# Performance work log

Measured on AMD Instinct MI355X. Metric: run time of the kernel, lower is better.

Reference implementation:

```python
import jax, jax.numpy as jnp
import numpy as np

IN, H1, H2, V = 1024, 2048, 2048, 50257


def setup_inputs() -> dict:
    key = jax.random.key(0)
    ks = jax.random.split(key, 16)
    def n(k, shape, scale=1.0):
        return (jax.random.normal(k, shape, dtype=jnp.float32) * scale).astype(jnp.float32)
    s1 = 1.0 / np.sqrt(H1)  # pytorch LSTM init scale ~ U(-1/sqrt(H),1/sqrt(H)); gaussian stand-in
    s2 = 1.0 / np.sqrt(H2)
    so = 1.0 / np.sqrt(H2)
    return {
        "x":  n(ks[0], (IN,)),
        "h1": n(ks[1], (H1,)), "c1": n(ks[2], (H1,)),
        "h2": n(ks[3], (H2,)), "c2": n(ks[4], (H2,)),
        "W_ih1": n(ks[5], (4 * H1, IN), s1), "W_hh1": n(ks[6], (4 * H1, H1), s1),
        "b_ih1": n(ks[7], (4 * H1,), s1),   "b_hh1": n(ks[8], (4 * H1,), s1),
        "W_ih2": n(ks[9], (4 * H2, H1), s2), "W_hh2": n(ks[10], (4 * H2, H2), s2),
        "b_ih2": n(ks[11], (4 * H2,), s2),  "b_hh2": n(ks[12], (4 * H2,), s2),
        "W_out": n(ks[13], (V, H2), so),    "b_out": n(ks[14], (V,), so),
    }


def _lstm_step(x, h, c, W_ih, W_hh, b_ih, b_hh):
    # PyTorch gate ordering: i, f, g, o
    gates = W_ih @ x + b_ih + W_hh @ h + b_hh  # [4H]
    i, f, g, o = jnp.split(gates, 4)
    i = jax.nn.sigmoid(i)
    f = jax.nn.sigmoid(f)
    g = jnp.tanh(g)
    o = jax.nn.sigmoid(o)
    c_new = f * c + i * g
    h_new = o * jnp.tanh(c_new)
    return h_new, c_new


def reference(x, h1, c1, h2, c2,
              W_ih1, W_hh1, b_ih1, b_hh1,
              W_ih2, W_hh2, b_ih2, b_hh2,
              W_out, b_out):
    h1n, _ = _lstm_step(x, h1, c1, W_ih1, W_hh1, b_ih1, b_hh1)
    h2n, _ = _lstm_step(h1n, h2, c2, W_ih2, W_hh2, b_ih2, b_hh2)
    logits = W_out @ h2n + b_out                     # [V]
    # dropout(p=0.1) treated as identity (eval mode) for a deterministic baseline
    return jax.nn.log_softmax(logits)[None, :]       # [1, V], matches dim=1 log-softmax
```

## Files before the change

### kernel.cpp

```cpp
#include <hip/hip_runtime.h>
#include <hip/hip_bf16.h>

typedef unsigned short u16;
typedef u16 u16x8 __attribute__((ext_vector_type(8)));
typedef float f32x8 __attribute__((ext_vector_type(8)));

#define IN_DIM 1024
#define H_DIM  2048
#define V_DIM  50257
#define NEG_BIG (-1e30f)

__device__ __forceinline__ float bf2f(u16 u) {
    union { unsigned int i; float f; } v;
    v.i = ((unsigned int)u) << 16;
    return v.f;
}

__device__ __forceinline__ u16 f2bf(float f) {
    union { float f; unsigned int i; } v;
    v.f = f;
    unsigned int i = v.i;
    i += 0x7fffu + ((i >> 16) & 1u);
    return (u16)(i >> 16);
}

__device__ __forceinline__ float wave_reduce_sum(float v) {
    #pragma unroll
    for (int off = 32; off > 0; off >>= 1) v += __shfl_down(v, off, 64);
    return v;
}

__device__ __forceinline__ float sigmoidf(float x) { return 1.f / (1.f + __expf(-x)); }

__device__ __forceinline__ float ld_scalar(const void* p, int i, bool bf) {
    return bf ? bf2f(((const u16*)p)[i]) : ((const float*)p)[i];
}

__device__ __forceinline__ const void* row_ptr(const void* W, size_t row, int n, bool bf) {
    return (const void*)((const char*)W + row * (size_t)n * (bf ? 2u : 4u));
}

template<int N>
__device__ __forceinline__ float dot_dt(const void* wrow, const void* v, int lane, bool bf) {
    float acc = 0.f;
    if (bf) {
        const u16x8* wp = (const u16x8*)wrow;
        const u16x8* vp = (const u16x8*)v;
        #pragma unroll
        for (int k = 0; k < N / 512; ++k) {
            u16x8 a = wp[lane + 64 * k];
            u16x8 b = vp[lane + 64 * k];
            #pragma unroll
            for (int t = 0; t < 8; ++t) acc += bf2f(a[t]) * bf2f(b[t]);
        }
    } else {
        const f32x8* wp = (const f32x8*)wrow;
        const f32x8* vp = (const f32x8*)v;
        #pragma unroll
        for (int k = 0; k < N / 512; ++k) {
            f32x8 a = wp[lane + 64 * k];
            f32x8 b = vp[lane + 64 * k];
            #pragma unroll
            for (int t = 0; t < 8; ++t) acc += a[t] * b[t];
        }
    }
    return acc;
}

template<int N>
__device__ __forceinline__ float dot_dt_f32v(const void* wrow, const float* v, int lane, bool bf) {
    float acc = 0.f;
    const f32x8* vp = (const f32x8*)v;
    if (bf) {
        const u16x8* wp = (const u16x8*)wrow;
        #pragma unroll
        for (int k = 0; k < N / 512; ++k) {
            u16x8 a = wp[lane + 64 * k];
            f32x8 b = vp[lane + 64 * k];
            #pragma unroll
            for (int t = 0; t < 8; ++t) acc += bf2f(a[t]) * b[t];
        }
    } else {
        const f32x8* wp = (const f32x8*)wrow;
        #pragma unroll
        for (int k = 0; k < N / 512; ++k) {
            f32x8 a = wp[lane + 64 * k];
            f32x8 b = vp[lane + 64 * k];
            #pragma unroll
            for (int t = 0; t < 8; ++t) acc += a[t] * b[t];
        }
    }
    return acc;
}

__global__ __launch_bounds__(64) void probe_kernel(const void* x, int* flag) {
    const int lane = threadIdx.x;
    const u16* p = (const u16*)x;
    int cnt = 0;
    #pragma unroll
    for (int k = 0; k < 8; ++k) {
        u16 w = p[2 * (lane + 64 * k)];
        int e = (w >> 7) & 0xFF;
        if (e >= 0x60 && e <= 0x8F) cnt++;
    }
    float c = wave_reduce_sum((float)cnt);
    if (lane == 0) flag[0] = (c > 300.f) ? 1 : 0;
}

__global__ __launch_bounds__(256) void lstm1_kernel(
    const void* __restrict__ x, const void* __restrict__ h1, const void* __restrict__ c1,
    const void* __restrict__ W_ih, const void* __restrict__ W_hh,
    const void* __restrict__ b_ih, const void* __restrict__ b_hh,
    const int* __restrict__ flag, float* __restrict__ h_out)
{
    const bool bf  = (*flag != 0);
    const int j    = blockIdx.x;
    const int wave = threadIdx.x >> 6;
    const int lane = threadIdx.x & 63;
    const int row  = wave * H_DIM + j;

    float acc = dot_dt<IN_DIM>(row_ptr(W_ih, (size_t)row, IN_DIM, bf), x, lane, bf)
              + dot_dt<H_DIM>(row_ptr(W_hh, (size_t)row, H_DIM, bf), h1, lane, bf);
    acc = wave_reduce_sum(acc);

    __shared__ float gs[4];
    if (lane == 0) gs[wave] = acc + ld_scalar(b_ih, row, bf) + ld_scalar(b_hh, row, bf);
    __syncthreads();
    if (threadIdx.x == 0) {
        float gi = sigmoidf(gs[0]);
        float gf = sigmoidf(gs[1]);
        float gg = tanhf(gs[2]);
        float go = sigmoidf(gs[3]);
        float c  = gf * ld_scalar(c1, j, bf) + gi * gg;
        h_out[j] = go * tanhf(c);
    }
}

__global__ __launch_bounds__(256) void lstm2_kernel(
    const float* __restrict__ h1n, const void* __restrict__ h2, const void* __restrict__ c2,
    const void* __restrict__ W_ih, const void* __restrict__ W_hh,
    const void* __restrict__ b_ih, const void* __restrict__ b_hh,
    const int* __restrict__ flag, float* __restrict__ h_out)
{
    const bool bf  = (*flag != 0);
    const int j    = blockIdx.x;
    const int wave = threadIdx.x >> 6;
    const int lane = threadIdx.x & 63;
    const int row  = wave * H_DIM + j;

    float acc = dot_dt_f32v<H_DIM>(row_ptr(W_ih, (size_t)row, H_DIM, bf), h1n, lane, bf)
              + dot_dt<H_DIM>(row_ptr(W_hh, (size_t)row, H_DIM, bf), h2, lane, bf);
    acc = wave_reduce_sum(acc);

    __shared__ float gs[4];
    if (lane == 0) gs[wave] = acc + ld_scalar(b_ih, row, bf) + ld_scalar(b_hh, row, bf);
    __syncthreads();
    if (threadIdx.x == 0) {
        float gi = sigmoidf(gs[0]);
        float gf = sigmoidf(gs[1]);
        float gg = tanhf(gs[2]);
        float go = sigmoidf(gs[3]);
        float c  = gf * ld_scalar(c2, j, bf) + gi * gg;
        h_out[j] = go * tanhf(c);
    }
}

#define ROWS_PER_WAVE 8
#define ROWS_PER_BLOCK 32
__global__ __launch_bounds__(256) void logits_kernel(
    const float* __restrict__ h2n, const void* __restrict__ W, const void* __restrict__ b,
    const int* __restrict__ flag,
    float* __restrict__ logits, float* __restrict__ pmax, float* __restrict__ psum)
{
    const bool bf  = (*flag != 0);
    const int wave = threadIdx.x >> 6;
    const int lane = threadIdx.x & 63;

    float hreg[32];
    {
        const f32x8* hv = (const f32x8*)h2n;
        #pragma unroll
        for (int k = 0; k < 4; ++k) {
            f32x8 hh = hv[lane + 64 * k];
            #pragma unroll
            for (int t = 0; t < 8; ++t) hreg[8 * k + t] = hh[t];
        }
    }

    const int base = blockIdx.x * ROWS_PER_BLOCK + wave * ROWS_PER_WAVE;
    float m = NEG_BIG, s = 0.f;
    for (int rr = 0; rr < ROWS_PER_WAVE; ++rr) {
        const int row = base + rr;
        if (row < V_DIM) {
            float acc = 0.f;
            if (bf) {
                const u16x8* wr = (const u16x8*)row_ptr(W, (size_t)row, H_DIM, true);
                #pragma unroll
                for (int k = 0; k < 4; ++k) {
                    u16x8 w = wr[lane + 64 * k];
                    #pragma unroll
                    for (int t = 0; t < 8; ++t) acc += bf2f(w[t]) * hreg[8 * k + t];
                }
            } else {
                const f32x8* wr = (const f32x8*)row_ptr(W, (size_t)row, H_DIM, false);
                #pragma unroll
                for (int k = 0; k < 4; ++k) {
                    f32x8 w = wr[lane + 64 * k];
                    #pragma unroll
                    for (int t = 0; t < 8; ++t) acc += w[t] * hreg[8 * k + t];
                }
            }
            acc = wave_reduce_sum(acc);
            if (lane == 0) {
                float lg = acc + ld_scalar(b, row, bf);
                logits[row] = lg;
                float mn = fmaxf(m, lg);
                s = s * __expf(m - mn) + __expf(lg - mn);
                m = mn;
            }
        }
    }
    __shared__ float wm[4], wsv[4];
    if (lane == 0) { wm[wave] = m; wsv[wave] = s; }
    __syncthreads();
    if (threadIdx.x == 0) {
        float M = fmaxf(fmaxf(wm[0], wm[1]), fmaxf(wm[2], wm[3]));
        float S = 0.f;
        #pragma unroll
        for (int w = 0; w < 4; ++w) S += wsv[w] * __expf(wm[w] - M);
        pmax[blockIdx.x] = M;
        psum[blockIdx.x] = S;
    }
}

__global__ __launch_bounds__(256) void finalize_kernel(
    const float* __restrict__ logits, const float* __restrict__ pmax,
    const float* __restrict__ psum, int nblk, const int* __restrict__ flag,
    void* __restrict__ out)
{
    const bool bf = (*flag != 0);
    __shared__ float sm[256], ss[256];
    float m = NEG_BIG, s = 0.f;
    for (int i = threadIdx.x; i < nblk; i += 256) {
        float bm = pmax[i], bs = psum[i];
        float mn = fmaxf(m, bm);
        s = s * __expf(m - mn) + bs * __expf(bm - mn);
        m = mn;
    }
    sm[threadIdx.x] = m; ss[threadIdx.x] = s;
    __syncthreads();
    #pragma unroll
    for (int stride = 128; stride > 0; stride >>= 1) {
        if ((int)threadIdx.x < stride) {
            float m1 = sm[threadIdx.x], s1 = ss[threadIdx.x];
            float m2 = sm[threadIdx.x + stride], s2 = ss[threadIdx.x + stride];
            float mn = fmaxf(m1, m2);
            sm[threadIdx.x] = mn;
            ss[threadIdx.x] = s1 * __expf(m1 - mn) + s2 * __expf(m2 - mn);
        }
        __syncthreads();
    }
    const float logZ = sm[0] + __logf(ss[0]);
    const int i = blockIdx.x * 256 + threadIdx.x;
    if (i < V_DIM) {
        float v = logits[i] - logZ;
        if (bf) ((u16*)out)[i] = f2bf(v);
        else    ((float*)out)[i] = v;
    }
}

extern "C" void kernel_launch(void* const* d_in, const int* in_sizes, int n_in,
                              void* d_out, int out_size, void* d_ws, size_t ws_size,
                              hipStream_t stream)
{
    const void* x     = d_in[0];
    const void* h1    = d_in[1];
    const void* c1    = d_in[2];
    const void* h2    = d_in[3];
    const void* c2    = d_in[4];
    const void* W_ih1 = d_in[5];
    const void* W_hh1 = d_in[6];
    const void* b_ih1 = d_in[7];
    const void* b_hh1 = d_in[8];
    const void* W_ih2 = d_in[9];
    const void* W_hh2 = d_in[10];
    const void* b_ih2 = d_in[11];
    const void* b_hh2 = d_in[12];
    const void* W_out = d_in[13];
    const void* b_out = d_in[14];

    float* ws     = (float*)d_ws;
    float* h1n    = ws;
    float* h2n    = ws + 2048;
    float* logits = ws + 4096;
    float* pmax   = ws + 4096 + 50264;
    float* psum   = pmax + 1576;
    int*   flag   = (int*)(psum + 1576);

    const int nblk3 = (V_DIM + ROWS_PER_BLOCK - 1) / ROWS_PER_BLOCK;

    probe_kernel<<<1, 64, 0, stream>>>(x, flag);
    lstm1_kernel<<<H_DIM, 256, 0, stream>>>(x, h1, c1, W_ih1, W_hh1, b_ih1, b_hh1, flag, h1n);
    lstm2_kernel<<<H_DIM, 256, 0, stream>>>(h1n, h2, c2, W_ih2, W_hh2, b_ih2, b_hh2, flag, h2n);
    logits_kernel<<<nblk3, 256, 0, stream>>>(h2n, W_out, b_out, flag, logits, pmax, psum);
    finalize_kernel<<<(V_DIM + 255) / 256, 256, 0, stream>>>(logits, pmax, psum, nblk3, flag, d_out);
}
```

Measured before the change: 679.0 us.

## Inline dtype probe, use nontemporal weight loads, batch two rows per wave in logits

Drops the separate probe kernel and has every block detect bf16 inline with a wave ballot, which saves one launch and the flag load that each kernel waited on. Weight rows are now read with nontemporal loads, all loads are issued before any math, and the logits kernel handles two rows per wave step with xor butterfly reductions so more memory requests are in flight. The row-bounds branches are replaced by clamped indices. The cost is a redundant probe read in every block, and the inline probe samples fewer elements, which makes the dtype guess less robust.

```diff
diff --git a/kernel.cpp b/kernel.cpp
--- a/kernel.cpp
+++ b/kernel.cpp
@@ -24,9 +24,12 @@
     return (u16)(i >> 16);
 }
 
-__device__ __forceinline__ float wave_reduce_sum(float v) {
+template<typename T>
+__device__ __forceinline__ T ntl(const T* p) { return __builtin_nontemporal_load(p); }
+
+__device__ __forceinline__ float wave_allreduce_sum(float v) {
     #pragma unroll
-    for (int off = 32; off > 0; off >>= 1) v += __shfl_down(v, off, 64);
+    for (int d = 32; d; d >>= 1) v += __shfl_xor(v, d, 64);
     return v;
 }
 
@@ -36,92 +39,76 @@
     return bf ? bf2f(((const u16*)p)[i]) : ((const float*)p)[i];
 }
 
-__device__ __forceinline__ const void* row_ptr(const void* W, size_t row, int n, bool bf) {
-    return (const void*)((const char*)W + row * (size_t)n * (bf ? 2u : 4u));
-}
-
-template<int N>
-__device__ __forceinline__ float dot_dt(const void* wrow, const void* v, int lane, bool bf) {
-    float acc = 0.f;
-    if (bf) {
-        const u16x8* wp = (const u16x8*)wrow;
-        const u16x8* vp = (const u16x8*)v;
-        #pragma unroll
-        for (int k = 0; k < N / 512; ++k) {
-            u16x8 a = wp[lane + 64 * k];
-            u16x8 b = vp[lane + 64 * k];
-            #pragma unroll
-            for (int t = 0; t < 8; ++t) acc += bf2f(a[t]) * bf2f(b[t]);
-        }
-    } else {
-        const f32x8* wp = (const f32x8*)wrow;
-        const f32x8* vp = (const f32x8*)v;
-        #pragma unroll
-        for (int k = 0; k < N / 512; ++k) {
-            f32x8 a = wp[lane + 64 * k];
-            f32x8 b = vp[lane + 64 * k];
-            #pragma unroll
-            for (int t = 0; t < 8; ++t) acc += a[t] * b[t];
-        }
-    }
-    return acc;
-}
-
-template<int N>
-__device__ __forceinline__ float dot_dt_f32v(const void* wrow, const float* v, int lane, bool bf) {
-    float acc = 0.f;
-    const f32x8* vp = (const f32x8*)v;
-    if (bf) {
-        const u16x8* wp = (const u16x8*)wrow;
-        #pragma unroll
-        for (int k = 0; k < N / 512; ++k) {
-            u16x8 a = wp[lane + 64 * k];
-            f32x8 b = vp[lane + 64 * k];
-            #pragma unroll
-            for (int t = 0; t < 8; ++t) acc += bf2f(a[t]) * b[t];
-        }
-    } else {
-        const f32x8* wp = (const f32x8*)wrow;
-        #pragma unroll
-        for (int k = 0; k < N / 512; ++k) {
-            f32x8 a = wp[lane + 64 * k];
-            f32x8 b = vp[lane + 64 * k];
-            #pragma unroll
-            for (int t = 0; t < 8; ++t) acc += a[t] * b[t];
-        }
-    }
-    return acc;
-}
-
-__global__ __launch_bounds__(64) void probe_kernel(const void* x, int* flag) {
-    const int lane = threadIdx.x;
+__device__ __forceinline__ bool probe_bf16(const void* x) {
     const u16* p = (const u16*)x;
-    int cnt = 0;
-    #pragma unroll
-    for (int k = 0; k < 8; ++k) {
-        u16 w = p[2 * (lane + 64 * k)];
-        int e = (w >> 7) & 0xFF;
-        if (e >= 0x60 && e <= 0x8F) cnt++;
-    }
-    float c = wave_reduce_sum((float)cnt);
-    if (lane == 0) flag[0] = (c > 300.f) ? 1 : 0;
+    const int lane = threadIdx.x & 63;
+    u16 w = p[2 * lane];
+    int e = (w >> 7) & 0xFF;
+    unsigned long long b = __ballot(e >= 0x60 && e <= 0x8F);
+    return __popcll(b) > 40;
 }
 
 __global__ __launch_bounds__(256) void lstm1_kernel(
     const void* __restrict__ x, const void* __restrict__ h1, const void* __restrict__ c1,
     const void* __restrict__ W_ih, const void* __restrict__ W_hh,
     const void* __restrict__ b_ih, const void* __restrict__ b_hh,
-    const int* __restrict__ flag, float* __restrict__ h_out)
-{
-    const bool bf  = (*flag != 0);
+    float* __restrict__ h_out)
+{
+    const bool bf  = probe_bf16(x);
     const int j    = blockIdx.x;
     const int wave = threadIdx.x >> 6;
     const int lane = threadIdx.x & 63;
     const int row  = wave * H_DIM + j;
 
-    float acc = dot_dt<IN_DIM>(row_ptr(W_ih, (size_t)row, IN_DIM, bf), x, lane, bf)
-              + dot_dt<H_DIM>(row_ptr(W_hh, (size_t)row, H_DIM, bf), h1, lane, bf);
-    acc = wave_reduce_sum(acc);
+    float acc = 0.f;
+    if (bf) {
+        {
+            const u16x8* wp = (const u16x8*)W_ih + (size_t)row * (IN_DIM / 8) + lane;
+            const u16x8* vp = (const u16x8*)x + lane;
+            u16x8 a[2], v[2];
+            #pragma unroll
+            for (int k = 0; k < 2; ++k) { a[k] = ntl(wp + 64 * k); v[k] = vp[64 * k]; }
+            #pragma unroll
+            for (int k = 0; k < 2; ++k)
+                #pragma unroll
+                for (int t = 0; t < 8; ++t) acc += bf2f(a[k][t]) * bf2f(v[k][t]);
+        }
+        {
+            const u16x8* wp = (const u16x8*)W_hh + (size_t)row * (H_DIM / 8) + lane;
+            const u16x8* vp = (const u16x8*)h1 + lane;
+            u16x8 a[4], v[4];
+            #pragma unroll
+            for (int k = 0; k < 4; ++k) { a[k] = ntl(wp + 64 * k); v[k] = vp[64 * k]; }
+            #pragma unroll
+            for (int k = 0; k < 4; ++k)
+                #pragma unroll
+                for (int t = 0; t < 8; ++t) acc += bf2f(a[k][t]) * bf2f(v[k][t]);
+        }
+    } else {
+        {
+            const f32x8* wp = (const f32x8*)W_ih + (size_t)row * (IN_DIM / 8) + lane;
+            const f32x8* vp = (const f32x8*)x + lane;
+            f32x8 a[2], v[2];
+            #pragma unroll
+            for (int k = 0; k < 2; ++k) { a[k] = ntl(wp + 64 * k); v[k] = vp[64 * k]; }
+            #pragma unroll
+            for (int k = 0; k < 2; ++k)
+                #pragma unroll
+                for (int t = 0; t < 8; ++t) acc += a[k][t] * v[k][t];
+        }
+        {
+            const f32x8* wp = (const f32x8*)W_hh + (size_t)row * (H_DIM / 8) + lane;
+            const f32x8* vp = (const f32x8*)h1 + lane;
+            f32x8 a[4], v[4];
+            #pragma unroll
+            for (int k = 0; k < 4; ++k) { a[k] = ntl(wp + 64 * k); v[k] = vp[64 * k]; }
+            #pragma unroll
+            for (int k = 0; k < 4; ++k)
+                #pragma unroll
+                for (int t = 0; t < 8; ++t) acc += a[k][t] * v[k][t];
+        }
+    }
+    acc = wave_allreduce_sum(acc);
 
     __shared__ float gs[4];
     if (lane == 0) gs[wave] = acc + ld_scalar(b_ih, row, bf) + ld_scalar(b_hh, row, bf);
@@ -137,20 +124,67 @@
 }
 
 __global__ __launch_bounds__(256) void lstm2_kernel(
+    const void* __restrict__ x,
     const float* __restrict__ h1n, const void* __restrict__ h2, const void* __restrict__ c2,
     const void* __restrict__ W_ih, const void* __restrict__ W_hh,
     const void* __restrict__ b_ih, const void* __restrict__ b_hh,
-    const int* __restrict__ flag, float* __restrict__ h_out)
-{
-    const bool bf  = (*flag != 0);
+    float* __restrict__ h_out)
+{
+    const bool bf  = probe_bf16(x);
     const int j    = blockIdx.x;
     const int wave = threadIdx.x >> 6;
     const int lane = threadIdx.x & 63;
     const int row  = wave * H_DIM + j;
 
-    float acc = dot_dt_f32v<H_DIM>(row_ptr(W_ih, (size_t)row, H_DIM, bf), h1n, lane, bf)
-              + dot_dt<H_DIM>(row_ptr(W_hh, (size_t)row, H_DIM, bf), h2, lane, bf);
-    acc = wave_reduce_sum(acc);
+    float acc = 0.f;
+    if (bf) {
+        {
+            const u16x8* wp = (const u16x8*)W_ih + (size_t)row * (H_DIM / 8) + lane;
+            const f32x8* vp = (const f32x8*)h1n + lane;
+            u16x8 a[4]; f32x8 v[4];
+            #pragma unroll
+            for (int k = 0; k < 4; ++k) { a[k] = ntl(wp + 64 * k); v[k] = vp[64 * k]; }
+            #pragma unroll
+            for (int k = 0; k < 4; ++k)
+                #pragma unroll
+                for (int t = 0; t < 8; ++t) acc += bf2f(a[k][t]) * v[k][t];
+        }
+        {
+            const u16x8* wp = (const u16x8*)W_hh + (size_t)row * (H_DIM / 8) + lane;
+            const u16x8* vp = (const u16x8*)h2 + lane;
+            u16x8 a[4], v[4];
+            #pragma unroll
+            for (int k = 0; k < 4; ++k) { a[k] = ntl(wp + 64 * k); v[k] = vp[64 * k]; }
+            #pragma unroll
+            for (int k = 0; k < 4; ++k)
+                #pragma unroll
+                for (int t = 0; t < 8; ++t) acc += bf2f(a[k][t]) * bf2f(v[k][t]);
+        }
+    } else {
+        {
+            const f32x8* wp = (const f32x8*)W_ih + (size_t)row * (H_DIM / 8) + lane;
+            const f32x8* vp = (const f32x8*)h1n + lane;
+            f32x8 a[4], v[4];
+            #pragma unroll
+            for (int k = 0; k < 4; ++k) { a[k] = ntl(wp + 64 * k); v[k] = vp[64 * k]; }
+            #pragma unroll
+            for (int k = 0; k < 4; ++k)
+                #pragma unroll
+                for (int t = 0; t < 8; ++t) acc += a[k][t] * v[k][t];
+        }
+        {
+            const f32x8* wp = (const f32x8*)W_hh + (size_t)row * (H_DIM / 8) + lane;
+            const f32x8* vp = (const f32x8*)h2 + lane;
+            f32x8 a[4], v[4];
+            #pragma unroll
+            for (int k = 0; k < 4; ++k) { a[k] = ntl(wp + 64 * k); v[k] = vp[64 * k]; }
+            #pragma unroll
+            for (int k = 0; k < 4; ++k)
+                #pragma unroll
+                for (int t = 0; t < 8; ++t) acc += a[k][t] * v[k][t];
+        }
+    }
+    acc = wave_allreduce_sum(acc);
 
     __shared__ float gs[4];
     if (lane == 0) gs[wave] = acc + ld_scalar(b_ih, row, bf) + ld_scalar(b_hh, row, bf);
@@ -168,11 +202,11 @@
 #define ROWS_PER_WAVE 8
 #define ROWS_PER_BLOCK 32
 __global__ __launch_bounds__(256) void logits_kernel(
+    const void* __restrict__ x,
     const float* __restrict__ h2n, const void* __restrict__ W, const void* __restrict__ b,
-    const int* __restrict__ flag,
     float* __restrict__ logits, float* __restrict__ pmax, float* __restrict__ psum)
 {
-    const bool bf  = (*flag != 0);
+    const bool bf  = probe_bf16(x);
     const int wave = threadIdx.x >> 6;
     const int lane = threadIdx.x & 63;
 
@@ -189,37 +223,73 @@
 
     const int base = blockIdx.x * ROWS_PER_BLOCK + wave * ROWS_PER_WAVE;
     float m = NEG_BIG, s = 0.f;
-    for (int rr = 0; rr < ROWS_PER_WAVE; ++rr) {
-        const int row = base + rr;
-        if (row < V_DIM) {
+
+    if (bf) {
+        #pragma unroll
+        for (int p = 0; p < 4; ++p) {
+            const int r0 = base + 2 * p, r1 = r0 + 1;
+            const int c0 = min(r0, V_DIM - 1), c1 = min(r1, V_DIM - 1);
+            const u16x8* w0 = (const u16x8*)W + (size_t)c0 * (H_DIM / 8) + lane;
+            const u16x8* w1 = (const u16x8*)W + (size_t)c1 * (H_DIM / 8) + lane;
+            u16x8 a0[4], a1[4];
+            #pragma unroll
+            for (int k = 0; k < 4; ++k) { a0[k] = ntl(w0 + 64 * k); a1[k] = ntl(w1 + 64 * k); }
+            float acc0 = 0.f, acc1 = 0.f;
+            #pragma unroll
+            for (int k = 0; k < 4; ++k)
+                #pragma unroll
+                for (int t = 0; t < 8; ++t) {
+                    float hval = hreg[8 * k + t];
+                    acc0 += bf2f(a0[k][t]) * hval;
+                    acc1 += bf2f(a1[k][t]) * hval;
+                }
+            #pragma unroll
+            for (int d = 32; d; d >>= 1) {
+                acc0 += __shfl_xor(acc0, d, 64);
+                acc1 += __shfl_xor(acc1, d, 64);
+            }
+            const float l0 = acc0 + ld_scalar(b, c0, true);
+            const float l1 = acc1 + ld_scalar(b, c1, true);
+            const bool v0 = (r0 < V_DIM), v1 = (r1 < V_DIM);
+            if (lane == 0) {
+                if (v0) logits[r0] = l0;
+                if (v1) logits[r1] = l1;
+            }
+            const float mx = fmaxf(v0 ? l0 : NEG_BIG, v1 ? l1 : NEG_BIG);
+            if (mx > -1e29f) {
+                const float mn = fmaxf(m, mx);
+                s = s * __expf(m - mn)
+                  + (v0 ? __expf(l0 - mn) : 0.f)
+                  + (v1 ? __expf(l1 - mn) : 0.f);
+                m = mn;
+            }
+        }
+    } else {
+        #pragma unroll
+        for (int rr = 0; rr < ROWS_PER_WAVE; ++rr) {
+            const int r = base + rr;
+            const int cr = min(r, V_DIM - 1);
+            const f32x8* wr = (const f32x8*)W + (size_t)cr * (H_DIM / 8) + lane;
+            f32x8 a[4];
+            #pragma unroll
+            for (int k = 0; k < 4; ++k) a[k] = ntl(wr + 64 * k);
             float acc = 0.f;
-            if (bf) {
-                const u16x8* wr = (const u16x8*)row_ptr(W, (size_t)row, H_DIM, true);
-                #pragma unroll
-                for (int k = 0; k < 4; ++k) {
-                    u16x8 w = wr[lane + 64 * k];
-                    #pragma unroll
-                    for (int t = 0; t < 8; ++t) acc += bf2f(w[t]) * hreg[8 * k + t];
-                }
-            } else {
-                const f32x8* wr = (const f32x8*)row_ptr(W, (size_t)row, H_DIM, false);
-                #pragma unroll
-                for (int k = 0; k < 4; ++k) {
-                    f32x8 w = wr[lane + 64 * k];
-                    #pragma unroll
-                    for (int t = 0; t < 8; ++t) acc += w[t] * hreg[8 * k + t];
-                }
-            }
-            acc = wave_reduce_sum(acc);
-            if (lane == 0) {
-                float lg = acc + ld_scalar(b, row, bf);
-                logits[row] = lg;
-                float mn = fmaxf(m, lg);
+            #pragma unroll
+            for (int k = 0; k < 4; ++k)
+                #pragma unroll
+                for (int t = 0; t < 8; ++t) acc += a[k][t] * hreg[8 * k + t];
+            acc = wave_allreduce_sum(acc);
+            const float lg = acc + ((const float*)b)[cr];
+            const bool v = (r < V_DIM);
+            if (lane == 0 && v) logits[r] = lg;
+            if (v) {
+                const float mn = fmaxf(m, lg);
                 s = s * __expf(m - mn) + __expf(lg - mn);
                 m = mn;
             }
         }
     }
+
     __shared__ float wm[4], wsv[4];
     if (lane == 0) { wm[wave] = m; wsv[wave] = s; }
     __syncthreads();
@@ -234,11 +304,12 @@
 }
 
 __global__ __launch_bounds__(256) void finalize_kernel(
+    const void* __restrict__ x,
     const float* __restrict__ logits, const float* __restrict__ pmax,
-    const float* __restrict__ psum, int nblk, const int* __restrict__ flag,
+    const float* __restrict__ psum, int nblk,
     void* __restrict__ out)
 {
-    const bool bf = (*flag != 0);
+    const bool bf = probe_bf16(x);
     __shared__ float sm[256], ss[256];
     float m = NEG_BIG, s = 0.f;
     for (int i = threadIdx.x; i < nblk; i += 256) {
@@ -295,13 +366,11 @@
     float* logits = ws + 4096;
     float* pmax   = ws + 4096 + 50264;
     float* psum   = pmax + 1576;
-    int*   flag   = (int*)(psum + 1576);
 
     const int nblk3 = (V_DIM + ROWS_PER_BLOCK - 1) / ROWS_PER_BLOCK;
 
-    probe_kernel<<<1, 64, 0, stream>>>(x, flag);
-    lstm1_kernel<<<H_DIM, 256, 0, stream>>>(x, h1, c1, W_ih1, W_hh1, b_ih1, b_hh1, flag, h1n);
-    lstm2_kernel<<<H_DIM, 256, 0, stream>>>(h1n, h2, c2, W_ih2, W_hh2, b_ih2, b_hh2, flag, h2n);
-    logits_kernel<<<nblk3, 256, 0, stream>>>(h2n, W_out, b_out, flag, logits, pmax, psum);
-    finalize_kernel<<<(V_DIM + 255) / 256, 256, 0, stream>>>(logits, pmax, psum, nblk3, flag, d_out);
-}
+    lstm1_kernel<<<H_DIM, 256, 0, stream>>>(x, h1, c1, W_ih1, W_hh1, b_ih1, b_hh1, h1n);
+    lstm2_kernel<<<H_DIM, 256, 0, stream>>>(x, h1n, h2, c2, W_ih2, W_hh2, b_ih2, b_hh2, h2n);
+    logits_kernel<<<nblk3, 256, 0, stream>>>(x, h2n, W_out, b_out, logits, pmax, psum);
+    finalize_kernel<<<(V_DIM + 255) / 256, 256, 0, stream>>>(x, logits, pmax, psum, nblk3, d_out);
+}
```

Result: no change. 685.3 us (+0.9%).
